# Kernel optimization log

Hardware: AMD Instinct MI355X
Metric: run time of the kernel (lower is better)

The kernel has to match this reference:

```python
import jax, jax.numpy as jnp
import numpy as np
import math

V, B, C, H, W = 4, 8, 512, 16, 16
NH = 8


def setup_inputs() -> dict:
    key = jax.random.key(0)
    ks = jax.random.split(key, 10)
    def n(k, shape, s=1.0):
        return jax.random.normal(k, shape, dtype=jnp.float32) * s
    return dict(
        i=n(ks[0], (V, B, C, H, W)),
        c=n(ks[1], (V, B, C, H, W)),
        j=n(ks[2], (V, B, C, H, W)),
        ln1_g=jnp.ones((C,), jnp.float32), ln1_b=jnp.zeros((C,), jnp.float32),
        ln2_g=jnp.ones((C,), jnp.float32), ln2_b=jnp.zeros((C,), jnp.float32),
        Wq=n(ks[3], (C, C), 0.02), bq=jnp.zeros((C,), jnp.float32),
        Wkv=n(ks[4], (C, 2 * C), 0.02), bkv=jnp.zeros((2 * C,), jnp.float32),
        Wo=n(ks[5], (C, C), 0.02), bo=jnp.zeros((C,), jnp.float32),
        Wfc=n(ks[6], (C, 4 * C), 0.02), bfc=jnp.zeros((4 * C,), jnp.float32),
        Wpr=n(ks[7], (4 * C, C), 0.02), bpr=jnp.zeros((C,), jnp.float32),
    )


def _ln(x, g, b, eps=1e-5):
    mu = jnp.mean(x, axis=-1, keepdims=True)
    var = jnp.mean((x - mu) ** 2, axis=-1, keepdims=True)
    return (x - mu) * jax.lax.rsqrt(var + eps) * g + b


def _gelu_new(x):
    # 0.5*x*(1+tanh(sqrt(2/pi)*(x+0.044715*x^3)))
    k = math.sqrt(2.0 / math.pi)
    return 0.5 * x * (1.0 + jnp.tanh(k * (x + 0.044715 * x ** 3)))


def reference(i, c, j, ln1_g, ln1_b, ln2_g, ln2_b, Wq, bq, Wkv, bkv, Wo, bo, Wfc, bfc, Wpr, bpr):
    v, b, ch, h, w = i.shape
    T = v * h * w
    hd = ch // NH

    def to_seq(x):  # v b c h w -> b (v h w) c
        return jnp.transpose(x, (1, 0, 3, 4, 2)).reshape(b, T, ch)

    # LayerNorm (over channel dim) applied before attention
    qs = _ln(to_seq(i), ln1_g, ln1_b)   # [b, T, c]
    kvs = _ln(to_seq(j), ln1_g, ln1_b)  # [b, T, c]

    q = qs @ Wq + bq                    # [b, T, c]
    kv = kvs @ Wkv + bkv                # [b, T, 2c]
    k, vv = jnp.split(kv, 2, axis=-1)

    def heads(x):  # [b, T, c] -> [b, nh, T, hd]
        return x.reshape(b, T, NH, hd).transpose(0, 2, 1, 3)
    q, k, vv = heads(q), heads(k), heads(vv)

    # block-causal mask: token in view-block r attends to view-blocks <= r
    blk = jnp.arange(T) // (h * w)
    mask = blk[:, None] >= blk[None, :]  # [T, T] bool

    att = jnp.einsum('bhqd,bhkd->bhqk', q, k) * (1.0 / math.sqrt(hd))
    att = jnp.where(mask, att, -jnp.inf)
    att = jax.nn.softmax(att, axis=-1)
    y = jnp.einsum('bhqk,bhkd->bhqd', att, vv)
    y = y.transpose(0, 2, 1, 3).reshape(b, T, ch)
    y = y @ Wo + bo                     # attention output, seq layout

    # residual: ln1(c) + attn
    cs = _ln(to_seq(c), ln1_g, ln1_b) + y
    # MLP with residual
    hcs = _ln(cs, ln2_g, ln2_b)
    cs = cs + (_gelu_new(hcs @ Wfc + bfc) @ Wpr + bpr)

    # b (v h w) c -> v b c h w
    out = cs.reshape(b, v, h, w, ch).transpose(1, 0, 4, 2, 3)
    return out
```

## Files before the change

kernel.cpp:

```cpp
#include <hip/hip_runtime.h>
#include <hip/hip_bf16.h>
#include <math.h>


typedef __bf16 bf16;
typedef __bf16 bf16x8 __attribute__((ext_vector_type(8)));
typedef __bf16 bf16x4 __attribute__((ext_vector_type(4)));
typedef float  f32x4  __attribute__((ext_vector_type(4)));

__device__ __forceinline__ void gload_lds16(const void* g, void* l) {
  __builtin_amdgcn_global_load_lds(
      (__attribute__((address_space(1))) void*)(g),
      (__attribute__((address_space(3))) void*)(l), 16, 0, 0);
}

__global__ __launch_bounds__(256)
void prep_k(const float* __restrict__ Wq, const float* __restrict__ Wkv,
            const float* __restrict__ Wo, const float* __restrict__ Wfc,
            const float* __restrict__ Wpr,
            bf16* __restrict__ WqT, bf16* __restrict__ WkvT,
            bf16* __restrict__ WoT, bf16* __restrict__ WfcT,
            bf16* __restrict__ WprT,
            const float* __restrict__ xi, const float* __restrict__ xj,
            const float* __restrict__ xc,
            const float* __restrict__ g, const float* __restrict__ bb,
            bf16* __restrict__ qs, bf16* __restrict__ kvs,
            bf16* __restrict__ csb)
{
  __shared__ float tile[64 * 65];
  __shared__ float red[4][64];
  const int t = blockIdx.x;
  const int tid = threadIdx.x;
  if (t < 768) {
    const float* W; bf16* Wt; int K, N, nx, tl;
    if (t < 64)        { W = Wq;  Wt = WqT;  K = 512;  N = 512;  nx = 8;  tl = t; }
    else if (t < 192)  { W = Wkv; Wt = WkvT; K = 512;  N = 1024; nx = 16; tl = t - 64; }
    else if (t < 256)  { W = Wo;  Wt = WoT;  K = 512;  N = 512;  nx = 8;  tl = t - 192; }
    else if (t < 512)  { W = Wfc; Wt = WfcT; K = 512;  N = 2048; nx = 32; tl = t - 256; }
    else               { W = Wpr; Wt = WprT; K = 2048; N = 512;  nx = 8;  tl = t - 512; }
    const int bx = tl % nx, by = tl / nx;
    const int n0 = bx << 6, k0 = by << 6;
    const int xl = tid & 15, yl = tid >> 4;
#pragma unroll
    for (int r = 0; r < 4; ++r) {
      const int row = yl + r * 16;
      const f32x4 vv = *(const f32x4*)&W[(size_t)(k0 + row) * N + n0 + xl * 4];
#pragma unroll
      for (int e = 0; e < 4; ++e)
        tile[row * 65 + xl * 4 + e] = vv[e];
    }
    __syncthreads();
    const int xk = tid & 7, nl = tid >> 3;
#pragma unroll
    for (int r2 = 0; r2 < 2; ++r2) {
      const int n = nl + r2 * 32;
      bf16x8 o;
#pragma unroll
      for (int e = 0; e < 8; ++e)
        o[e] = (bf16)tile[(xk * 8 + e) * 65 + n];
      *(bf16x8*)&Wt[(size_t)(n0 + n) * K + k0 + xk * 8] = o;
    }
    return;
  }
  const int u = t - 768;
  const int sel = u >> 8, bid = u & 255;
  const int b = bid & 7, hp = (bid >> 3) & 7, v = bid >> 6;
  const float* src = (sel == 0) ? xi : ((sel == 1) ? xj : xc);
  const size_t base = ((size_t)(v * 8 + b) * 512) * 256 + hp * 32;
  const int q8 = tid & 7, chb = tid >> 3;
  const int wid = tid >> 6, lc = (tid >> 3) & 7;
  const int cb = chb << 4;

  float gr[16], br[16];
#pragma unroll
  for (int p = 0; p < 4; ++p) {
    *(f32x4*)&gr[p * 4] = *(const f32x4*)&g[cb + p * 4];
    *(f32x4*)&br[p * 4] = *(const f32x4*)&bb[cb + p * 4];
  }
  f32x4 x[16];
#pragma unroll
  for (int k = 0; k < 16; ++k)
    x[k] = *(const f32x4*)&src[base + (size_t)(cb + k) * 256 + q8 * 4];

  float s[4] = {0.f, 0.f, 0.f, 0.f}, ss[4] = {0.f, 0.f, 0.f, 0.f};
#pragma unroll
  for (int k = 0; k < 16; ++k)
#pragma unroll
    for (int i = 0; i < 4; ++i) {
      s[i] += x[k][i];
      ss[i] += x[k][i] * x[k][i];
    }
#pragma unroll
  for (int off = 8; off < 64; off <<= 1)
#pragma unroll
    for (int i = 0; i < 4; ++i) {
      s[i] += __shfl_xor(s[i], off);
      ss[i] += __shfl_xor(ss[i], off);
    }
  if (lc < 4)      red[wid][q8 * 4 + lc]            = s[lc];
  else             red[wid][32 + q8 * 4 + (lc - 4)] = ss[lc - 4];
  __syncthreads();
  f32x4 st = {0.f, 0.f, 0.f, 0.f}, sst = {0.f, 0.f, 0.f, 0.f};
#pragma unroll
  for (int w = 0; w < 4; ++w) {
    st  += *(const f32x4*)&red[w][q8 * 4];
    sst += *(const f32x4*)&red[w][32 + q8 * 4];
  }
  float mu[4], rs[4];
#pragma unroll
  for (int i = 0; i < 4; ++i) {
    mu[i] = st[i] * (1.f / 512.f);
    rs[i] = rsqrtf(sst[i] * (1.f / 512.f) - mu[i] * mu[i] + 1e-5f);
  }
  bf16* dstb = (sel == 0) ? qs : ((sel == 1) ? kvs : csb);
  const int tkb = v * 256 + hp * 32 + q8 * 4;
#pragma unroll
  for (int i = 0; i < 4; ++i) {
    const size_t orow = ((size_t)b * 1024 + tkb + i) * 512 + cb;
    bf16x8 o0, o1;
#pragma unroll
    for (int k = 0; k < 8; ++k) {
      o0[k] = (bf16)((x[k][i] - mu[i]) * rs[i] * gr[k] + br[k]);
      o1[k] = (bf16)((x[k + 8][i] - mu[i]) * rs[i] * gr[k + 8] + br[k + 8]);
    }
    *(bf16x8*)&dstb[orow]     = o0;
    *(bf16x8*)&dstb[orow + 8] = o1;
  }
}

__global__ __launch_bounds__(256)
void ln2_k(const bf16* __restrict__ cs, const float* __restrict__ g,
           const float* __restrict__ bb, bf16* __restrict__ hcs)
{
  const int tid = threadIdx.x, wid = tid >> 6, lane = tid & 63;
  const int bid = blockIdx.x;
  const int xcd = bid & 7, c2 = bid >> 3;
  const int row = xcd * 1024 + c2 * 4 + wid;
  const bf16x8 v8 = *(const bf16x8*)&cs[(size_t)row * 512 + lane * 8];
  float v[8];
#pragma unroll
  for (int k = 0; k < 8; ++k) v[k] = (float)v8[k];
  float s = 0.f, ss = 0.f;
#pragma unroll
  for (int k = 0; k < 8; ++k) { s += v[k]; ss += v[k] * v[k]; }
#pragma unroll
  for (int off = 1; off < 64; off <<= 1) {
    s += __shfl_xor(s, off);
    ss += __shfl_xor(ss, off);
  }
  const float mu = s * (1.f / 512.f);
  const float rstd = rsqrtf(ss * (1.f / 512.f) - mu * mu + 1e-5f);
  bf16x8 o;
#pragma unroll
  for (int k = 0; k < 8; ++k) {
    int ch = lane * 8 + k;
    o[k] = (bf16)((v[k] - mu) * rstd * g[ch] + bb[ch]);
  }
  *(bf16x8*)&hcs[(size_t)row * 512 + lane * 8] = o;
}

__global__ __launch_bounds__(512)
void gemm_fc_k(const bf16* __restrict__ A, const bf16* __restrict__ Bt,
               const float* __restrict__ bias, bf16* __restrict__ fo)
{
  const int K = 512;
  __shared__ __align__(16) char smem[69632];
  bf16* As = (bf16*)smem;
  bf16* Bs = (bf16*)(smem + 16384);
  bf16* OT = (bf16*)smem;
  const int tid = threadIdx.x;
  const int wid = tid >> 6, lane = tid & 63;
  const int wr = wid >> 2, wcc = wid & 3;
  const int ml = lane & 15, kg = (lane >> 4) << 3;
  const int bid = blockIdx.x;
  const int xcd = bid & 7, chunk = bid >> 3;
  const int m0 = (xcd * 8 + (chunk & 7)) * 128;
  const int n0 = (chunk >> 3) * 256;

  const int rA = (wid << 4) + (lane >> 2), cA = (lane & 3) << 3;
  const bf16* Ag = A + (size_t)m0 * K;
  const bf16* Bg = Bt + (size_t)n0 * K;

  f32x4 acc[4][4] = {};

  gload_lds16(Ag + (size_t)rA * K + cA,         As + wid * 512);
  gload_lds16(Bg + (size_t)rA * K + cA,         Bs + wid * 512);
  gload_lds16(Bg + (size_t)(rA + 128) * K + cA, Bs + 4096 + wid * 512);

  int cur = 0;
  for (int k0 = 0; k0 < K; k0 += 32) {
    __syncthreads();
    if (k0 + 32 < K) {
      const int nb = cur ^ 1, kn = k0 + 32;
      gload_lds16(Ag + (size_t)rA * K + kn + cA,         As + nb * 4096 + wid * 512);
      gload_lds16(Bg + (size_t)rA * K + kn + cA,         Bs + nb * 8192 + wid * 512);
      gload_lds16(Bg + (size_t)(rA + 128) * K + kn + cA, Bs + nb * 8192 + 4096 + wid * 512);
    }
    bf16x8 af[4], bfr[4];
#pragma unroll
    for (int mf = 0; mf < 4; ++mf)
      af[mf] = *(const bf16x8*)&As[cur * 4096 + (wr * 64 + mf * 16 + ml) * 32 + kg];
#pragma unroll
    for (int nf = 0; nf < 4; ++nf)
      bfr[nf] = *(const bf16x8*)&Bs[cur * 8192 + (wcc * 64 + nf * 16 + ml) * 32 + kg];
#pragma unroll
    for (int mf = 0; mf < 4; ++mf)
#pragma unroll
      for (int nf = 0; nf < 4; ++nf)
        acc[mf][nf] = __builtin_amdgcn_mfma_f32_16x16x32_bf16(
            af[mf], bfr[nf], acc[mf][nf], 0, 0, 0);
    cur ^= 1;
  }

  __syncthreads();
  const int jrow0 = (lane >> 4) << 2;
#pragma unroll
  for (int nf = 0; nf < 4; ++nf) {
    const float bv = bias[n0 + wcc * 64 + nf * 16 + ml];
#pragma unroll
    for (int mf = 0; mf < 4; ++mf)
#pragma unroll
      for (int j = 0; j < 4; ++j) {
        float x = acc[mf][nf][j] + bv;
        float u = 0.7978845608f * (x + 0.044715f * x * x * x);
        float e = __expf(2.f * u);
        float th = 1.f - 2.f / (e + 1.f);
        OT[(wr * 64 + mf * 16 + jrow0 + j) * 264 + wcc * 64 + nf * 16 + ml] =
            (bf16)(0.5f * x * (1.f + th));
      }
  }
  __syncthreads();
#pragma unroll
  for (int it = 0; it < 8; ++it) {
    const int idx = it * 512 + tid;
    const int cg = idx & 31, r = idx >> 5;
    *(bf16x8*)&fo[(size_t)(m0 + r) * 2048 + n0 + cg * 8] =
        *(const bf16x8*)&OT[r * 264 + cg * 8];
  }
}

enum { EPI_O = 2, EPI_PR = 4 };

template <int EPI>
__global__ __launch_bounds__(512)
void gemmsk_k(const bf16* __restrict__ A, const bf16* __restrict__ Bt,
              const float* __restrict__ bias, const bf16* res,
              void* out0, int K)
{
  __shared__ __align__(16) char smem[49152];
  bf16*  AS = (bf16*)smem;
  bf16*  BS = (bf16*)(smem + 16384);
  float* CF = (float*)smem;

  const int tid = threadIdx.x;
  const int wid = tid >> 6, lane = tid & 63;
  const int half = wid >> 2, w2 = wid & 3;
  const int wr = w2 >> 1, wc = w2 & 1;
  const int ml = lane & 15, kg = (lane >> 4) << 3;
  const int bid = blockIdx.x;
  const int xcd = bid & 7, chunk = bid >> 3;
  const int m0 = (xcd * 16 + (chunk & 15)) * 64;
  const int n0 = (chunk >> 4) * 128;
  const int Kh = K >> 1;

  const int eA = w2 * 512 + lane * 8;
  const int rA = eA >> 5, cA = eA & 31;
  const int eB0 = (w2 * 2) * 512 + lane * 8;
  const int rB0 = eB0 >> 5, cB0 = eB0 & 31;
  const int eB1 = eB0 + 512;
  const int rB1 = eB1 >> 5, cB1 = eB1 & 31;

  const bf16* Ag = A + (size_t)m0 * K + half * Kh;
  const bf16* Bg = Bt + (size_t)n0 * K + half * Kh;

  f32x4 acc[2][4] = {};

  gload_lds16(Ag + (size_t)rA * K + cA, AS + half * 2048 + w2 * 512);
  gload_lds16(Bg + (size_t)rB0 * K + cB0, BS + half * 4096 + (w2 * 2) * 512);
  gload_lds16(Bg + (size_t)rB1 * K + cB1, BS + half * 4096 + (w2 * 2 + 1) * 512);

  int cur = 0;
  for (int k0 = 0; k0 < Kh; k0 += 32) {
    __syncthreads();
    if (k0 + 32 < Kh) {
      const int kn = k0 + 32, nb = cur ^ 1;
      gload_lds16(Ag + (size_t)rA * K + kn + cA,
                  AS + nb * 4096 + half * 2048 + w2 * 512);
      gload_lds16(Bg + (size_t)rB0 * K + kn + cB0,
                  BS + nb * 8192 + half * 4096 + (w2 * 2) * 512);
      gload_lds16(Bg + (size_t)rB1 * K + kn + cB1,
                  BS + nb * 8192 + half * 4096 + (w2 * 2 + 1) * 512);
    }
    const bf16* Ac = AS + cur * 4096 + half * 2048;
    const bf16* Bc = BS + cur * 8192 + half * 4096;
    bf16x8 af[2], bfr[4];
#pragma unroll
    for (int mf = 0; mf < 2; ++mf)
      af[mf] = *(const bf16x8*)&Ac[(wr * 32 + mf * 16 + ml) * 32 + kg];
#pragma unroll
    for (int nf = 0; nf < 4; ++nf)
      bfr[nf] = *(const bf16x8*)&Bc[(wc * 64 + nf * 16 + ml) * 32 + kg];
#pragma unroll
    for (int mf = 0; mf < 2; ++mf)
#pragma unroll
      for (int nf = 0; nf < 4; ++nf)
        acc[mf][nf] = __builtin_amdgcn_mfma_f32_16x16x32_bf16(
            af[mf], bfr[nf], acc[mf][nf], 0, 0, 0);
    cur ^= 1;
  }

  const int jrow0 = (lane >> 4) << 2;
  __syncthreads();
  if (half == 0) {
#pragma unroll
    for (int mf = 0; mf < 2; ++mf)
#pragma unroll
      for (int nf = 0; nf < 4; ++nf)
#pragma unroll
        for (int j = 0; j < 4; ++j)
          CF[(wr * 32 + mf * 16 + jrow0 + j) * 128 + wc * 64 + nf * 16 + ml] =
              acc[mf][nf][j];
  }
  __syncthreads();
  if (half == 1) {
#pragma unroll
    for (int nf = 0; nf < 4; ++nf) {
      const int n = n0 + wc * 64 + nf * 16 + ml;
      const float bv = bias[n];
#pragma unroll
      for (int mf = 0; mf < 2; ++mf) {
        const int mbase = m0 + wr * 32 + mf * 16 + jrow0;
        float v4[4];
#pragma unroll
        for (int j = 0; j < 4; ++j)
          v4[j] = acc[mf][nf][j] +
                  CF[(wr * 32 + mf * 16 + jrow0 + j) * 128 + wc * 64 + nf * 16 + ml];
        if constexpr (EPI == EPI_O) {
          bf16* cs = (bf16*)out0;
#pragma unroll
          for (int j = 0; j < 4; ++j) {
            const size_t idx = (size_t)(mbase + j) * 512 + n;
            cs[idx] = (bf16)(v4[j] + bv + (float)res[idx]);
          }
        } else {
          float* out = (float*)out0;
          const int b = mbase >> 10, t = mbase & 1023;
          const int v = t >> 8, hhh = (t >> 4) & 15, w0 = t & 15;
          f32x4 o;
#pragma unroll
          for (int j = 0; j < 4; ++j)
            o[j] = v4[j] + bv + (float)res[(size_t)(mbase + j) * 512 + n];
          *(f32x4*)&out[(((size_t)v * 8 + b) * 512 + n) * 256 + hhh * 16 + w0] = o;
        }
      }
    }
  }
}

__global__ __launch_bounds__(256)
void gemm_qkv_k(const bf16* __restrict__ Aq, const bf16* __restrict__ Akv,
                const bf16* __restrict__ WqT, const bf16* __restrict__ WkvT,
                const float* __restrict__ bq, const float* __restrict__ bkv,
                bf16* __restrict__ q_buf, bf16* __restrict__ k_buf,
                bf16* __restrict__ v_t)
{
  const int K = 512;
  __shared__ __align__(16) char smem[34816];
  bf16* As = (bf16*)smem;
  bf16* Bs = (bf16*)(smem + 16384);
  const int tid = threadIdx.x;
  const int wid = tid >> 6, lane = tid & 63;
  const int wr = wid >> 1, wc = wid & 1;
  const int ml = lane & 15, kg = (lane >> 4) << 3;
  const int bid = blockIdx.x;
  const int xcd = bid & 7, chunk = bid >> 3;
  const int m0 = (xcd * 8 + (chunk & 7)) * 128;
  const int ybl = chunk >> 3;
  const bool isq = ybl < 4;
  const bf16* A     = isq ? Aq  : Akv;
  const bf16* Bt    = isq ? WqT : WkvT;
  const float* bias = isq ? bq : bkv;
  const int n0 = isq ? (ybl << 7) : ((ybl - 4) << 7);

  const int e0 = wid * 512 + lane * 8;
  const int r0 = e0 >> 5, c0 = e0 & 31;
  const int e1 = e0 + 2048;
  const int r1 = e1 >> 5, c1 = e1 & 31;

  const bf16* Ag = A + (size_t)m0 * K;
  const bf16* Bg = Bt + (size_t)n0 * K;

  f32x4 acc[4][4] = {};

  gload_lds16(Ag + (size_t)r0 * K + c0, As + wid * 512);
  gload_lds16(Ag + (size_t)r1 * K + c1, As + 2048 + wid * 512);
  gload_lds16(Bg + (size_t)r0 * K + c0, Bs + wid * 512);
  gload_lds16(Bg + (size_t)r1 * K + c1, Bs + 2048 + wid * 512);

  int cur = 0;
  for (int k0 = 0; k0 < K; k0 += 32) {
    __syncthreads();
    if (k0 + 32 < K) {
      const int nb = cur ^ 1, kn = k0 + 32;
      gload_lds16(Ag + (size_t)r0 * K + kn + c0, As + nb * 4096 + wid * 512);
      gload_lds16(Ag + (size_t)r1 * K + kn + c1, As + nb * 4096 + 2048 + wid * 512);
      gload_lds16(Bg + (size_t)r0 * K + kn + c0, Bs + nb * 4096 + wid * 512);
      gload_lds16(Bg + (size_t)r1 * K + kn + c1, Bs + nb * 4096 + 2048 + wid * 512);
    }
    bf16x8 af[4], bfr[4];
#pragma unroll
    for (int mf = 0; mf < 4; ++mf)
      af[mf] = *(const bf16x8*)&As[cur * 4096 + (wr * 64 + mf * 16 + ml) * 32 + kg];
#pragma unroll
    for (int nf = 0; nf < 4; ++nf)
      bfr[nf] = *(const bf16x8*)&Bs[cur * 4096 + (wc * 64 + nf * 16 + ml) * 32 + kg];
#pragma unroll
    for (int mf = 0; mf < 4; ++mf)
#pragma unroll
      for (int nf = 0; nf < 4; ++nf)
        acc[mf][nf] = __builtin_amdgcn_mfma_f32_16x16x32_bf16(
            af[mf], bfr[nf], acc[mf][nf], 0, 0, 0);
    cur ^= 1;
  }

  __syncthreads();
  bf16* OT = (bf16*)smem;
  const int jrow0 = (lane >> 4) << 2;
  const int b = m0 >> 10, t0 = m0 & 1023;
  if (ybl < 8) {
#pragma unroll
    for (int nf = 0; nf < 4; ++nf) {
      const float bv = bias[n0 + wc * 64 + nf * 16 + ml];
#pragma unroll
      for (int mf = 0; mf < 4; ++mf)
#pragma unroll
        for (int j = 0; j < 4; ++j)
          OT[(wr * 64 + mf * 16 + jrow0 + j) * 132 + wc * 64 + nf * 16 + ml] =
              (bf16)(acc[mf][nf][j] + bv);
    }
    __syncthreads();
    bf16* dst = isq ? q_buf : k_buf;
    const int h0 = n0 >> 6;
#pragma unroll
    for (int it = 0; it < 8; ++it) {
      const int idx = it * 256 + tid;
      const int dg = idx & 7, r = (idx >> 3) & 127, hl = idx >> 10;
      *(bf16x8*)&dst[(((size_t)b * 8 + h0 + hl) * 1024 + t0 + r) * 64 + dg * 8] =
          *(const bf16x8*)&OT[r * 132 + hl * 64 + dg * 8];
    }
  } else {
#pragma unroll
    for (int nf = 0; nf < 4; ++nf) {
      const float bv = bias[n0 + wc * 64 + nf * 16 + ml];
#pragma unroll
      for (int mf = 0; mf < 4; ++mf) {
        bf16x4 o;
#pragma unroll
        for (int j = 0; j < 4; ++j) o[j] = (bf16)(acc[mf][nf][j] + bv);
        *(bf16x4*)&OT[(wc * 64 + nf * 16 + ml) * 132 + wr * 64 + mf * 16 + jrow0] = o;
      }
    }
    __syncthreads();
    const int h0 = (n0 - 512) >> 6;
#pragma unroll
    for (int it = 0; it < 8; ++it) {
      const int idx = it * 256 + tid;
      const int og = idx & 15, c = idx >> 4;
      const int hl = c >> 6, d = c & 63;
      *(bf16x8*)&v_t[(((size_t)b * 8 + h0 + hl) * 64 + d) * 1024 + t0 + og * 8] =
          *(const bf16x8*)&OT[c * 132 + og * 8];
    }
  }
}

__global__ __launch_bounds__(512)
void attn_k(const bf16* __restrict__ qb, const bf16* __restrict__ kb,
            const bf16* __restrict__ vt, bf16* __restrict__ y)
{
  __shared__ bf16 Ks[2][4096];
  __shared__ bf16 Vs[2][4096];
  __shared__ bf16 Ps[8][1024];
  const int tid = threadIdx.x, wid = tid >> 6, lane = tid & 63;
  const int L = blockIdx.x;
  const int xcd = L & 7, chunk = L >> 3;
  const int bh = (xcd << 3) + (chunk >> 3);
  const int qt = 7 - (chunk & 7);
  const int b = bh >> 3, h = bh & 7;
  const int t0 = qt << 7;
  const int ml = lane & 15, hi = lane >> 4, kg = hi << 3;

  const bf16* qrow = qb + ((size_t)bh * 1024 + t0 + wid * 16) * 64;
  bf16x8 aq[2];
  aq[0] = *(const bf16x8*)&qrow[ml * 64 + kg];
  aq[1] = *(const bf16x8*)&qrow[ml * 64 + 32 + kg];

  f32x4 accO[4] = {};
  float lsum[4] = {0.f, 0.f, 0.f, 0.f};

  const int nkt = ((qt >> 1) + 1) << 2;
  const bf16* kbase = kb + (size_t)bh * 1024 * 64;
  const bf16* vbase = vt + (size_t)bh * 64 * 1024;

  const int sr = tid >> 3;
  const int sg = ((tid & 7) ^ (sr & 7)) << 3;
  bf16* pw = &Ps[wid][0];

  gload_lds16(kbase + (size_t)sr * 64 + sg,   &Ks[0][wid * 512]);
  gload_lds16(vbase + (size_t)sr * 1024 + sg, &Vs[0][wid * 512]);

  int cur = 0;
  for (int kt = 0; kt < nkt; ++kt) {
    __syncthreads();
    if (kt + 1 < nkt) {
      const int tk0 = (kt + 1) << 6;
      const int nb = cur ^ 1;
      gload_lds16(kbase + (size_t)(tk0 + sr) * 64 + sg,   &Ks[nb][wid * 512]);
      gload_lds16(vbase + (size_t)sr * 1024 + tk0 + sg,   &Vs[nb][wid * 512]);
    }

    f32x4 sa[4] = {};
    __builtin_amdgcn_s_setprio(1);
#pragma unroll
    for (int nf = 0; nf < 4; ++nf) {
      const int row = nf * 16 + ml;
#pragma unroll
      for (int ks = 0; ks < 2; ++ks) {
        const int g = ((ks * 4 + hi) ^ (ml & 7)) << 3;
        bf16x8 bk = *(const bf16x8*)&Ks[cur][row * 64 + g];
        sa[nf] = __builtin_amdgcn_mfma_f32_16x16x32_bf16(aq[ks], bk, sa[nf], 0, 0, 0);
      }
    }
    __builtin_amdgcn_s_setprio(0);

#pragma unroll
    for (int nf = 0; nf < 4; ++nf) {
      const int gp0 = nf * 2 + (ml >> 3);
#pragma unroll
      for (int j = 0; j < 4; ++j) {
        const float p = __expf(sa[nf][j] * 0.125f);
        lsum[j] += p;
        const int prow = (hi << 2) + j;
        pw[prow * 64 + ((gp0 ^ (prow & 7)) << 3) + (ml & 7)] = (bf16)p;
      }
    }

    __builtin_amdgcn_s_setprio(1);
#pragma unroll
    for (int ks = 0; ks < 2; ++ks) {
      const int g = ((ks * 4 + hi) ^ (ml & 7)) << 3;
      bf16x8 pa = *(const bf16x8*)&pw[ml * 64 + g];
#pragma unroll
      for (int df = 0; df < 4; ++df) {
        bf16x8 bv = *(const bf16x8*)&Vs[cur][(df * 16 + ml) * 64 + g];
        accO[df] = __builtin_amdgcn_mfma_f32_16x16x32_bf16(pa, bv, accO[df], 0, 0, 0);
      }
    }
    __builtin_amdgcn_s_setprio(0);
    cur ^= 1;
  }

  float inv[4];
#pragma unroll
  for (int j = 0; j < 4; ++j) {
    float s = lsum[j];
#pragma unroll
    for (int off = 1; off < 16; off <<= 1) s += __shfl_xor(s, off);
    inv[j] = 1.f / s;
  }
#pragma unroll
  for (int df = 0; df < 4; ++df)
#pragma unroll
    for (int j = 0; j < 4; ++j) {
      const int t = t0 + wid * 16 + (hi << 2) + j;
      const int c = h * 64 + df * 16 + ml;
      y[((size_t)b * 1024 + t) * 512 + c] = (bf16)(accO[df][j] * inv[j]);
    }
}

extern "C" void kernel_launch(void* const* d_in, const int* in_sizes, int n_in,
                              void* d_out, int out_size, void* d_ws, size_t ws_size,
                              hipStream_t stream)
{
  const float* xi    = (const float*)d_in[0];
  const float* xc    = (const float*)d_in[1];
  const float* xj    = (const float*)d_in[2];
  const float* ln1_g = (const float*)d_in[3];
  const float* ln1_b = (const float*)d_in[4];
  const float* ln2_g = (const float*)d_in[5];
  const float* ln2_b = (const float*)d_in[6];
  const float* Wq    = (const float*)d_in[7];
  const float* bq    = (const float*)d_in[8];
  const float* Wkv   = (const float*)d_in[9];
  const float* bkv   = (const float*)d_in[10];
  const float* Wo    = (const float*)d_in[11];
  const float* bo    = (const float*)d_in[12];
  const float* Wfc   = (const float*)d_in[13];
  const float* bfc   = (const float*)d_in[14];
  const float* Wpr   = (const float*)d_in[15];
  const float* bpr   = (const float*)d_in[16];

  char* ws = (char*)d_ws;
  const size_t MB = 1ull << 20;
  bf16*  qs    = (bf16*)(ws + 0);
  bf16*  kvs   = (bf16*)(ws + 8 * MB);
  bf16*  csb   = (bf16*)(ws + 16 * MB);
  bf16*  WqT   = (bf16*)(ws + 32 * MB);
  bf16*  WkvT  = (bf16*)(ws + 32 * MB + 512 * 1024);
  bf16*  WoT   = (bf16*)(ws + 33 * MB + 512 * 1024);
  bf16*  WfcT  = (bf16*)(ws + 34 * MB);
  bf16*  WprT  = (bf16*)(ws + 36 * MB);
  bf16*  q_buf = (bf16*)(ws + 38 * MB);
  bf16*  k_buf = (bf16*)(ws + 46 * MB);
  bf16*  v_t   = (bf16*)(ws + 54 * MB);
  bf16*  yb    = (bf16*)(ws + 0);
  bf16*  hcs   = (bf16*)(ws + 8 * MB);
  bf16*  fcact = (bf16*)(ws + 38 * MB);

  prep_k<<<dim3(1536), 256, 0, stream>>>(Wq, Wkv, Wo, Wfc, Wpr,
                                         WqT, WkvT, WoT, WfcT, WprT,
                                         xi, xj, xc, ln1_g, ln1_b, qs, kvs, csb);

  gemm_qkv_k<<<dim3(768), 256, 0, stream>>>(qs, kvs, WqT, WkvT, bq, bkv,
                                            q_buf, k_buf, v_t);

  attn_k<<<dim3(512), 512, 0, stream>>>(q_buf, k_buf, v_t, yb);

  gemmsk_k<EPI_O><<<dim3(512), 512, 0, stream>>>(yb, WoT, bo, csb,
                                                 (void*)csb, 512);

  ln2_k<<<dim3(2048), 256, 0, stream>>>(csb, ln2_g, ln2_b, hcs);

  gemm_fc_k<<<dim3(512), 512, 0, stream>>>(hcs, WfcT, bfc, fcact);

  gemmsk_k<EPI_PR><<<dim3(512), 512, 0, stream>>>(fcact, WprT, bpr, csb,
                                                  d_out, 2048);

  (void)in_sizes; (void)n_in; (void)out_size; (void)ws_size;
}
```

Measured before the change: 153.9 us.

## Triple-buffer GEMM K-loops with explicit vmcnt waits and raw barriers

Converts the double-buffered LDS pipelines in the FC, split-K output/projection, and QKV GEMM kernels to three stages, prefetching two K-tiles ahead. Each iteration waits with an explicit s_waitcnt vmcnt that lets the newest stage stay in flight, followed by a raw s_barrier, instead of a full __syncthreads that drains every outstanding load. This is meant to hide global-to-LDS latency better. In exchange LDS use grows per block (up to 72KB), which may lower occupancy, and correctness now depends on the hand-set vmcnt counts matching the loads issued per stage.

New measurement: 150.1 us. -2.5%, faster.

```diff
diff --git a/kernel.cpp b/kernel.cpp
--- a/kernel.cpp
+++ b/kernel.cpp
@@ -13,6 +13,14 @@
       (__attribute__((address_space(1))) void*)(g),
       (__attribute__((address_space(3))) void*)(l), 16, 0, 0);
 }
+
+#define VM_FENCE(N)                                              \
+  do {                                                           \
+    asm volatile("s_waitcnt vmcnt(" #N ")" ::: "memory");        \
+    __builtin_amdgcn_sched_barrier(0);                           \
+    __builtin_amdgcn_s_barrier();                                \
+    __builtin_amdgcn_sched_barrier(0);                           \
+  } while (0)
 
 __global__ __launch_bounds__(256)
 void prep_k(const float* __restrict__ Wq, const float* __restrict__ Wkv,
@@ -164,9 +172,9 @@
                const float* __restrict__ bias, bf16* __restrict__ fo)
 {
   const int K = 512;
-  __shared__ __align__(16) char smem[69632];
+  __shared__ __align__(16) char smem[73728];
   bf16* As = (bf16*)smem;
-  bf16* Bs = (bf16*)(smem + 16384);
+  bf16* Bs = (bf16*)(smem + 24576);
   bf16* OT = (bf16*)smem;
   const int tid = threadIdx.x;
   const int wid = tid >> 6, lane = tid & 63;
@@ -183,19 +191,20 @@
 
   f32x4 acc[4][4] = {};
 
-  gload_lds16(Ag + (size_t)rA * K + cA,         As + wid * 512);
-  gload_lds16(Bg + (size_t)rA * K + cA,         Bs + wid * 512);
-  gload_lds16(Bg + (size_t)(rA + 128) * K + cA, Bs + 4096 + wid * 512);
-
-  int cur = 0;
-  for (int k0 = 0; k0 < K; k0 += 32) {
-    __syncthreads();
-    if (k0 + 32 < K) {
-      const int nb = cur ^ 1, kn = k0 + 32;
-      gload_lds16(Ag + (size_t)rA * K + kn + cA,         As + nb * 4096 + wid * 512);
-      gload_lds16(Bg + (size_t)rA * K + kn + cA,         Bs + nb * 8192 + wid * 512);
-      gload_lds16(Bg + (size_t)(rA + 128) * K + kn + cA, Bs + nb * 8192 + 4096 + wid * 512);
-    }
+#define FC_STAGE(kk, bu)                                                      \
+  do {                                                                        \
+    gload_lds16(Ag + (size_t)rA * K + (kk) + cA,         As + (bu) * 4096 + wid * 512); \
+    gload_lds16(Bg + (size_t)rA * K + (kk) + cA,         Bs + (bu) * 8192 + wid * 512); \
+    gload_lds16(Bg + (size_t)(rA + 128) * K + (kk) + cA, Bs + (bu) * 8192 + 4096 + wid * 512); \
+  } while (0)
+
+  FC_STAGE(0, 0);
+  FC_STAGE(32, 1);
+
+  for (int kt = 0; kt < 16; ++kt) {
+    if (kt == 15) VM_FENCE(0); else VM_FENCE(3);
+    if (kt + 2 < 16) FC_STAGE((kt + 2) * 32, (kt + 2) % 3);
+    const int cur = kt % 3;
     bf16x8 af[4], bfr[4];
 #pragma unroll
     for (int mf = 0; mf < 4; ++mf)
@@ -209,8 +218,8 @@
       for (int nf = 0; nf < 4; ++nf)
         acc[mf][nf] = __builtin_amdgcn_mfma_f32_16x16x32_bf16(
             af[mf], bfr[nf], acc[mf][nf], 0, 0, 0);
-    cur ^= 1;
-  }
+  }
+#undef FC_STAGE
 
   __syncthreads();
   const int jrow0 = (lane >> 4) << 2;
@@ -247,9 +256,9 @@
               const float* __restrict__ bias, const bf16* res,
               void* out0, int K)
 {
-  __shared__ __align__(16) char smem[49152];
+  __shared__ __align__(16) char smem[73728];
   bf16*  AS = (bf16*)smem;
-  bf16*  BS = (bf16*)(smem + 16384);
+  bf16*  BS = (bf16*)(smem + 24576);
   float* CF = (float*)smem;
 
   const int tid = threadIdx.x;
@@ -262,6 +271,7 @@
   const int m0 = (xcd * 16 + (chunk & 15)) * 64;
   const int n0 = (chunk >> 4) * 128;
   const int Kh = K >> 1;
+  const int NK = Kh >> 5;
 
   const int eA = w2 * 512 + lane * 8;
   const int rA = eA >> 5, cA = eA & 31;
@@ -275,22 +285,20 @@
 
   f32x4 acc[2][4] = {};
 
-  gload_lds16(Ag + (size_t)rA * K + cA, AS + half * 2048 + w2 * 512);
-  gload_lds16(Bg + (size_t)rB0 * K + cB0, BS + half * 4096 + (w2 * 2) * 512);
-  gload_lds16(Bg + (size_t)rB1 * K + cB1, BS + half * 4096 + (w2 * 2 + 1) * 512);
-
-  int cur = 0;
-  for (int k0 = 0; k0 < Kh; k0 += 32) {
-    __syncthreads();
-    if (k0 + 32 < Kh) {
-      const int kn = k0 + 32, nb = cur ^ 1;
-      gload_lds16(Ag + (size_t)rA * K + kn + cA,
-                  AS + nb * 4096 + half * 2048 + w2 * 512);
-      gload_lds16(Bg + (size_t)rB0 * K + kn + cB0,
-                  BS + nb * 8192 + half * 4096 + (w2 * 2) * 512);
-      gload_lds16(Bg + (size_t)rB1 * K + kn + cB1,
-                  BS + nb * 8192 + half * 4096 + (w2 * 2 + 1) * 512);
-    }
+#define SK_STAGE(kk, bu)                                                      \
+  do {                                                                        \
+    gload_lds16(Ag + (size_t)rA * K + (kk) + cA,   AS + (bu) * 4096 + half * 2048 + w2 * 512); \
+    gload_lds16(Bg + (size_t)rB0 * K + (kk) + cB0, BS + (bu) * 8192 + half * 4096 + (w2 * 2) * 512); \
+    gload_lds16(Bg + (size_t)rB1 * K + (kk) + cB1, BS + (bu) * 8192 + half * 4096 + (w2 * 2 + 1) * 512); \
+  } while (0)
+
+  SK_STAGE(0, 0);
+  SK_STAGE(32, 1);
+
+  for (int kt = 0; kt < NK; ++kt) {
+    if (kt == NK - 1) VM_FENCE(0); else VM_FENCE(3);
+    if (kt + 2 < NK) SK_STAGE((kt + 2) * 32, (kt + 2) % 3);
+    const int cur = kt % 3;
     const bf16* Ac = AS + cur * 4096 + half * 2048;
     const bf16* Bc = BS + cur * 8192 + half * 4096;
     bf16x8 af[2], bfr[4];
@@ -306,8 +314,8 @@
       for (int nf = 0; nf < 4; ++nf)
         acc[mf][nf] = __builtin_amdgcn_mfma_f32_16x16x32_bf16(
             af[mf], bfr[nf], acc[mf][nf], 0, 0, 0);
-    cur ^= 1;
-  }
+  }
+#undef SK_STAGE
 
   const int jrow0 = (lane >> 4) << 2;
   __syncthreads();
@@ -365,9 +373,9 @@
                 bf16* __restrict__ v_t)
 {
   const int K = 512;
-  __shared__ __align__(16) char smem[34816];
+  __shared__ __align__(16) char smem[49152];
   bf16* As = (bf16*)smem;
-  bf16* Bs = (bf16*)(smem + 16384);
+  bf16* Bs = (bf16*)(smem + 24576);
   const int tid = threadIdx.x;
   const int wid = tid >> 6, lane = tid & 63;
   const int wr = wid >> 1, wc = wid & 1;
@@ -392,21 +400,21 @@
 
   f32x4 acc[4][4] = {};
 
-  gload_lds16(Ag + (size_t)r0 * K + c0, As + wid * 512);
-  gload_lds16(Ag + (size_t)r1 * K + c1, As + 2048 + wid * 512);
-  gload_lds16(Bg + (size_t)r0 * K + c0, Bs + wid * 512);
-  gload_lds16(Bg + (size_t)r1 * K + c1, Bs + 2048 + wid * 512);
-
-  int cur = 0;
-  for (int k0 = 0; k0 < K; k0 += 32) {
-    __syncthreads();
-    if (k0 + 32 < K) {
-      const int nb = cur ^ 1, kn = k0 + 32;
-      gload_lds16(Ag + (size_t)r0 * K + kn + c0, As + nb * 4096 + wid * 512);
-      gload_lds16(Ag + (size_t)r1 * K + kn + c1, As + nb * 4096 + 2048 + wid * 512);
-      gload_lds16(Bg + (size_t)r0 * K + kn + c0, Bs + nb * 4096 + wid * 512);
-      gload_lds16(Bg + (size_t)r1 * K + kn + c1, Bs + nb * 4096 + 2048 + wid * 512);
-    }
+#define QKV_STAGE(kk, bu)                                                     \
+  do {                                                                        \
+    gload_lds16(Ag + (size_t)r0 * K + (kk) + c0, As + (bu) * 4096 + wid * 512); \
+    gload_lds16(Ag + (size_t)r1 * K + (kk) + c1, As + (bu) * 4096 + 2048 + wid * 512); \
+    gload_lds16(Bg + (size_t)r0 * K + (kk) + c0, Bs + (bu) * 4096 + wid * 512); \
+    gload_lds16(Bg + (size_t)r1 * K + (kk) + c1, Bs + (bu) * 4096 + 2048 + wid * 512); \
+  } while (0)
+
+  QKV_STAGE(0, 0);
+  QKV_STAGE(32, 1);
+
+  for (int kt = 0; kt < 16; ++kt) {
+    if (kt == 15) VM_FENCE(0); else VM_FENCE(4);
+    if (kt + 2 < 16) QKV_STAGE((kt + 2) * 32, (kt + 2) % 3);
+    const int cur = kt % 3;
     bf16x8 af[4], bfr[4];
 #pragma unroll
     for (int mf = 0; mf < 4; ++mf)
@@ -420,8 +428,8 @@
       for (int nf = 0; nf < 4; ++nf)
         acc[mf][nf] = __builtin_amdgcn_mfma_f32_16x16x32_bf16(
             af[mf], bfr[nf], acc[mf][nf], 0, 0, 0);
-    cur ^= 1;
-  }
+  }
+#undef QKV_STAGE
 
   __syncthreads();
   bf16* OT = (bf16*)smem;
```
